# Kernel tuning notes

Measured on AMD Instinct MI355X. Metric: run time of the kernel, lower is better.

## Reference

```python
import jax, jax.numpy as jnp
import numpy as np

B, E, H = 16384, 1024, 1024


def setup_inputs() -> dict:
    key = jax.random.key(0)
    ks = jax.random.split(key, 8)
    s = 1.0 / np.sqrt(H)
    return {
        "x": jax.random.normal(ks[0], (B, E), dtype=jnp.float32),
        "h": jax.random.normal(ks[1], (B, H), dtype=jnp.float32),
        "W_ri": jax.random.normal(ks[2], (E, H), dtype=jnp.float32) * s,
        "b_ri": jnp.zeros((H,), dtype=jnp.float32),
        "W_rh": jax.random.normal(ks[3], (H, H), dtype=jnp.float32) * s,
        "W_zi": jax.random.normal(ks[4], (E, H), dtype=jnp.float32) * s,
        "b_zi": jnp.zeros((H,), dtype=jnp.float32),
        "W_zh": jax.random.normal(ks[5], (H, H), dtype=jnp.float32) * s,
        "W_hi": jax.random.normal(ks[6], (E, H), dtype=jnp.float32) * s,
        "b_hi": jnp.zeros((H,), dtype=jnp.float32),
        "W_hh": jax.random.normal(ks[7], (H, H), dtype=jnp.float32) * s,
    }


def reference(x, h, W_ri, b_ri, W_rh, W_zi, b_zi, W_zh, W_hi, b_hi, W_hh):
    # GRU cell: r/z gates then candidate htilde, then blend.
    rt = jax.nn.sigmoid(x @ W_ri + b_ri + h @ W_rh)          # [B,H]
    zt = jax.nn.sigmoid(x @ W_zi + b_zi + h @ W_zh)          # [B,H]
    htilde = jnp.tanh(x @ W_hi + b_hi + (h * rt) @ W_hh)     # [B,H]
    h_new = (1.0 - zt) * h + zt * htilde                     # [B,H]
    # dp_keep_prob=1.0 -> dropout is identity; module returns (dropout(h), h)
    return h_new
```

## Files before the change

kernel.cpp:

```cpp
#include <hip/hip_runtime.h>


typedef short bf16x8 __attribute__((ext_vector_type(8)));
typedef float f32x4 __attribute__((ext_vector_type(4)));

static __device__ __forceinline__ unsigned short f2bf(float f) {
    unsigned int u = __float_as_uint(f);
    unsigned int r = (u + 0x7fffu + ((u >> 16) & 1u)) >> 16;
    return (unsigned short)r;
}

__global__ void cast_f32_bf16(const float* __restrict__ src,
                              unsigned short* __restrict__ dst, int n) {
    int i = (blockIdx.x * blockDim.x + threadIdx.x) * 4;
    if (i < n) {
        float4 v = *(const float4*)(src + i);
        ushort4 o;
        o.x = f2bf(v.x); o.y = f2bf(v.y); o.z = f2bf(v.z); o.w = f2bf(v.w);
        *(ushort4*)(dst + i) = o;
    }
}

__global__ void transpose_cast(const float* __restrict__ src,
                               unsigned short* __restrict__ dst,
                               int dst_col_off) {
    __shared__ float t[32][33];
    int bx = blockIdx.x, by = blockIdx.y;
    int tx = threadIdx.x, ty = threadIdx.y;
#pragma unroll
    for (int i = 0; i < 4; ++i)
        t[ty + 8 * i][tx] = src[(by * 32 + ty + 8 * i) * 1024 + bx * 32 + tx];
    __syncthreads();
#pragma unroll
    for (int i = 0; i < 4; ++i) {
        int n = bx * 32 + ty + 8 * i;
        int k = by * 32 + tx;
        dst[n * 2048 + dst_col_off + k] = f2bf(t[tx][ty + 8 * i]);
    }
}

template <int MODE>
__global__ void gemm_gru(const unsigned short* __restrict__ Alo,
                         const unsigned short* __restrict__ Ahi,
                         const unsigned short* __restrict__ Bt,
                         const float* __restrict__ bias,
                         const float* __restrict__ h,
                         float* __restrict__ zt,
                         unsigned short* __restrict__ ab,
                         float* __restrict__ out) {
    __shared__ __attribute__((aligned(16))) short As[128 * 32];
    __shared__ __attribute__((aligned(16))) short Bs[128 * 32];

    const int t = threadIdx.x;
    const int lane = t & 63;
    const int wave = t >> 6;
    const int bm = blockIdx.x >> 3;
    const int bn = blockIdx.x & 7;
    const int wm = wave >> 1, wn = wave & 1;

    f32x4 acc[4][4] = {};

    const int rowA0 = bm * 128;
    const int rowB0 = bn * 128;
    const int koff = (lane >> 4) * 8;
    const int rsub = lane & 15;

    for (int k0 = 0; k0 < 2048; k0 += 32) {
        const unsigned short* Asrc = (k0 < 1024)
            ? (Alo + rowA0 * 1024 + k0)
            : (Ahi + rowA0 * 1024 + (k0 - 1024));
        const unsigned short* Bsrc = Bt + rowB0 * 2048 + k0;

        __syncthreads();
#pragma unroll
        for (int j = 0; j < 2; ++j) {
            int c = j * 256 + wave * 64 + lane;
            int row = c >> 2;
            int part = c & 3;
            __builtin_amdgcn_global_load_lds(
                (const __attribute__((address_space(1))) void*)(Asrc + row * 1024 + part * 8),
                (__attribute__((address_space(3))) void*)(As + (j * 256 + wave * 64) * 8),
                16, 0, 0);
            __builtin_amdgcn_global_load_lds(
                (const __attribute__((address_space(1))) void*)(Bsrc + row * 2048 + part * 8),
                (__attribute__((address_space(3))) void*)(Bs + (j * 256 + wave * 64) * 8),
                16, 0, 0);
        }
        __syncthreads();

        bf16x8 af[4], bfr[4];
#pragma unroll
        for (int mi = 0; mi < 4; ++mi)
            af[mi] = *(const bf16x8*)(As + (wm * 64 + mi * 16 + rsub) * 32 + koff);
#pragma unroll
        for (int ni = 0; ni < 4; ++ni)
            bfr[ni] = *(const bf16x8*)(Bs + (wn * 64 + ni * 16 + rsub) * 32 + koff);
#pragma unroll
        for (int mi = 0; mi < 4; ++mi)
#pragma unroll
            for (int ni = 0; ni < 4; ++ni)
                acc[mi][ni] = __builtin_amdgcn_mfma_f32_16x16x32_bf16(
                    af[mi], bfr[ni], acc[mi][ni], 0, 0, 0);
    }

    const int q = lane >> 4;
#pragma unroll
    for (int mi = 0; mi < 4; ++mi) {
#pragma unroll
        for (int ni = 0; ni < 4; ++ni) {
            int col = bn * 128 + wn * 64 + ni * 16 + rsub;
            int row0 = bm * 128 + wm * 64 + mi * 16 + q * 4;
            float bz = bias[col];
#pragma unroll
            for (int r = 0; r < 4; ++r) {
                int idx = (row0 + r) * 1024 + col;
                float v = acc[mi][ni][r] + bz;
                if (MODE == 0) {
                    zt[idx] = 1.0f / (1.0f + __expf(-v));
                } else if (MODE == 1) {
                    float rt = 1.0f / (1.0f + __expf(-v));
                    ab[idx] = f2bf(h[idx] * rt);
                } else {
                    float ht = tanhf(v);
                    float hv = h[idx];
                    float z = zt[idx];
                    out[idx] = fmaf(z, ht - hv, hv);
                }
            }
        }
    }
}

extern "C" void kernel_launch(void* const* d_in, const int* in_sizes, int n_in,
                              void* d_out, int out_size, void* d_ws, size_t ws_size,
                              hipStream_t stream) {
    const float* x    = (const float*)d_in[0];
    const float* h    = (const float*)d_in[1];
    const float* W_ri = (const float*)d_in[2];
    const float* b_ri = (const float*)d_in[3];
    const float* W_rh = (const float*)d_in[4];
    const float* W_zi = (const float*)d_in[5];
    const float* b_zi = (const float*)d_in[6];
    const float* W_zh = (const float*)d_in[7];
    const float* W_hi = (const float*)d_in[8];
    const float* b_hi = (const float*)d_in[9];
    const float* W_hh = (const float*)d_in[10];
    float* out = (float*)d_out;

    const size_t MB = 1024ull * 1024ull;
    char* ws = (char*)d_ws;
    unsigned short* xb  = (unsigned short*)(ws);
    unsigned short* hb  = (unsigned short*)(ws + 32 * MB);
    unsigned short* ab  = (unsigned short*)(ws + 64 * MB);
    unsigned short* WrT = (unsigned short*)(ws + 96 * MB);
    unsigned short* WzT = (unsigned short*)(ws + 100 * MB);
    unsigned short* WhT = (unsigned short*)(ws + 104 * MB);
    float* zt = (float*)(ws + 108 * MB);

    const int NELEM = 16384 * 1024;
    cast_f32_bf16<<<NELEM / (256 * 4), 256, 0, stream>>>(x, xb, NELEM);
    cast_f32_bf16<<<NELEM / (256 * 4), 256, 0, stream>>>(h, hb, NELEM);

    dim3 tb(32, 8), tg(32, 32);
    transpose_cast<<<tg, tb, 0, stream>>>(W_ri, WrT, 0);
    transpose_cast<<<tg, tb, 0, stream>>>(W_rh, WrT, 1024);
    transpose_cast<<<tg, tb, 0, stream>>>(W_zi, WzT, 0);
    transpose_cast<<<tg, tb, 0, stream>>>(W_zh, WzT, 1024);
    transpose_cast<<<tg, tb, 0, stream>>>(W_hi, WhT, 0);
    transpose_cast<<<tg, tb, 0, stream>>>(W_hh, WhT, 1024);

    gemm_gru<0><<<1024, 256, 0, stream>>>(xb, hb, WzT, b_zi, h, zt, nullptr, nullptr);
    gemm_gru<1><<<1024, 256, 0, stream>>>(xb, hb, WrT, b_ri, h, nullptr, ab, nullptr);
    gemm_gru<2><<<1024, 256, 0, stream>>>(xb, ab, WhT, b_hi, h, zt, nullptr, out);
}
```

Before: 553.3 us.

## Fuse z and r gate GEMMs with 128x256 tiles and grouped block scheduling

Merges the z and r gate GEMMs into one GEMM over a concatenated 2048-wide weight, widens the block tile to 128x256, and reorders blocks into groups of 8 M-tiles so they share B tiles. Also merges the two cast kernels and the six transpose kernels into single launches. z is now stored as bf16, r*h is computed from bf16 h, and tanh is replaced by an exp-based formula. These cut launch count, A-matrix rereads and intermediate traffic, at the cost of more registers per thread (32 accumulators) and slightly lower precision.

After: 497.5 us. -10.1%, faster.

```diff
diff --git a/kernel.cpp b/kernel.cpp
--- a/kernel.cpp
+++ b/kernel.cpp
@@ -6,25 +6,36 @@
 
 static __device__ __forceinline__ unsigned short f2bf(float f) {
     unsigned int u = __float_as_uint(f);
-    unsigned int r = (u + 0x7fffu + ((u >> 16) & 1u)) >> 16;
-    return (unsigned short)r;
-}
-
-__global__ void cast_f32_bf16(const float* __restrict__ src,
-                              unsigned short* __restrict__ dst, int n) {
+    return (unsigned short)((u + 0x7fffu + ((u >> 16) & 1u)) >> 16);
+}
+static __device__ __forceinline__ float bf2f(unsigned short s) {
+    return __uint_as_float(((unsigned int)s) << 16);
+}
+
+__global__ void cast2_f32_bf16(const float* __restrict__ a,
+                               const float* __restrict__ b,
+                               unsigned short* __restrict__ da,
+                               unsigned short* __restrict__ db, int n) {
     int i = (blockIdx.x * blockDim.x + threadIdx.x) * 4;
-    if (i < n) {
-        float4 v = *(const float4*)(src + i);
-        ushort4 o;
-        o.x = f2bf(v.x); o.y = f2bf(v.y); o.z = f2bf(v.z); o.w = f2bf(v.w);
-        *(ushort4*)(dst + i) = o;
-    }
-}
-
-__global__ void transpose_cast(const float* __restrict__ src,
-                               unsigned short* __restrict__ dst,
-                               int dst_col_off) {
+    const float* s;
+    unsigned short* d;
+    int off;
+    if (i < n) { s = a; d = da; off = i; }
+    else       { s = b; d = db; off = i - n; }
+    float4 v = *(const float4*)(s + off);
+    ushort4 o;
+    o.x = f2bf(v.x); o.y = f2bf(v.y); o.z = f2bf(v.z); o.w = f2bf(v.w);
+    *(ushort4*)(d + off) = o;
+}
+
+struct TPlan {
+    const float* src[6];
+    unsigned short* dst[6];
+};
+__global__ void transpose_cast6(TPlan p) {
     __shared__ float t[32][33];
+    const float* src = p.src[blockIdx.z];
+    unsigned short* dst = p.dst[blockIdx.z];
     int bx = blockIdx.x, by = blockIdx.y;
     int tx = threadIdx.x, ty = threadIdx.y;
 #pragma unroll
@@ -35,35 +46,52 @@
     for (int i = 0; i < 4; ++i) {
         int n = bx * 32 + ty + 8 * i;
         int k = by * 32 + tx;
-        dst[n * 2048 + dst_col_off + k] = f2bf(t[tx][ty + 8 * i]);
+        dst[n * 2048 + k] = f2bf(t[tx][ty + 8 * i]);
     }
 }
 
-template <int MODE>
-__global__ void gemm_gru(const unsigned short* __restrict__ Alo,
-                         const unsigned short* __restrict__ Ahi,
-                         const unsigned short* __restrict__ Bt,
-                         const float* __restrict__ bias,
-                         const float* __restrict__ h,
-                         float* __restrict__ zt,
-                         unsigned short* __restrict__ ab,
-                         float* __restrict__ out) {
+template <int MODE, int NBN_LOG>
+__global__ __launch_bounds__(256, 2)
+void gemm_gru(const unsigned short* __restrict__ Alo,
+              const unsigned short* __restrict__ Ahi,
+              const unsigned short* __restrict__ Bt,
+              const float* __restrict__ bias_z,
+              const float* __restrict__ bias_r,
+              const unsigned short* __restrict__ hb,
+              const unsigned short* __restrict__ ztb_in,
+              const float* __restrict__ hf,
+              unsigned short* __restrict__ ztb_out,
+              unsigned short* __restrict__ ab_out,
+              float* __restrict__ out) {
+    constexpr int NBN = 1 << NBN_LOG;
     __shared__ __attribute__((aligned(16))) short As[128 * 32];
-    __shared__ __attribute__((aligned(16))) short Bs[128 * 32];
+    __shared__ __attribute__((aligned(16))) short Bs[256 * 32];
 
     const int t = threadIdx.x;
     const int lane = t & 63;
     const int wave = t >> 6;
-    const int bm = blockIdx.x >> 3;
-    const int bn = blockIdx.x & 7;
+    const int i = blockIdx.x;
+    const int bml = i & 7;
+    const int bn = (i >> 3) & (NBN - 1);
+    const int bmg = i >> (3 + NBN_LOG);
+    const int bm = bmg * 8 + bml;
     const int wm = wave >> 1, wn = wave & 1;
 
-    f32x4 acc[4][4] = {};
+    f32x4 acc[4][8] = {};
 
     const int rowA0 = bm * 128;
-    const int rowB0 = bn * 128;
+    const int rowB0 = bn * 256;
     const int koff = (lane >> 4) * 8;
     const int rsub = lane & 15;
+
+    const short* Ap[4];
+    const short* Bp[8];
+#pragma unroll
+    for (int mi = 0; mi < 4; ++mi)
+        Ap[mi] = As + (wm * 64 + mi * 16 + rsub) * 32 + koff;
+#pragma unroll
+    for (int ni = 0; ni < 8; ++ni)
+        Bp[ni] = Bs + (wn * 128 + ni * 16 + rsub) * 32 + koff;
 
     for (int k0 = 0; k0 < 2048; k0 += 32) {
         const unsigned short* Asrc = (k0 < 1024)
@@ -75,12 +103,16 @@
 #pragma unroll
         for (int j = 0; j < 2; ++j) {
             int c = j * 256 + wave * 64 + lane;
-            int row = c >> 2;
-            int part = c & 3;
+            int row = c >> 2, part = c & 3;
             __builtin_amdgcn_global_load_lds(
                 (const __attribute__((address_space(1))) void*)(Asrc + row * 1024 + part * 8),
                 (__attribute__((address_space(3))) void*)(As + (j * 256 + wave * 64) * 8),
                 16, 0, 0);
+        }
+#pragma unroll
+        for (int j = 0; j < 4; ++j) {
+            int c = j * 256 + wave * 64 + lane;
+            int row = c >> 2, part = c & 3;
             __builtin_amdgcn_global_load_lds(
                 (const __attribute__((address_space(1))) void*)(Bsrc + row * 2048 + part * 8),
                 (__attribute__((address_space(3))) void*)(Bs + (j * 256 + wave * 64) * 8),
@@ -88,17 +120,15 @@
         }
         __syncthreads();
 
-        bf16x8 af[4], bfr[4];
+        bf16x8 af[4], bfr[8];
+#pragma unroll
+        for (int mi = 0; mi < 4; ++mi) af[mi] = *(const bf16x8*)Ap[mi];
+#pragma unroll
+        for (int ni = 0; ni < 8; ++ni) bfr[ni] = *(const bf16x8*)Bp[ni];
 #pragma unroll
         for (int mi = 0; mi < 4; ++mi)
-            af[mi] = *(const bf16x8*)(As + (wm * 64 + mi * 16 + rsub) * 32 + koff);
-#pragma unroll
-        for (int ni = 0; ni < 4; ++ni)
-            bfr[ni] = *(const bf16x8*)(Bs + (wn * 64 + ni * 16 + rsub) * 32 + koff);
-#pragma unroll
-        for (int mi = 0; mi < 4; ++mi)
-#pragma unroll
-            for (int ni = 0; ni < 4; ++ni)
+#pragma unroll
+            for (int ni = 0; ni < 8; ++ni)
                 acc[mi][ni] = __builtin_amdgcn_mfma_f32_16x16x32_bf16(
                     af[mi], bfr[ni], acc[mi][ni], 0, 0, 0);
     }
@@ -107,23 +137,32 @@
 #pragma unroll
     for (int mi = 0; mi < 4; ++mi) {
 #pragma unroll
-        for (int ni = 0; ni < 4; ++ni) {
-            int col = bn * 128 + wn * 64 + ni * 16 + rsub;
+        for (int ni = 0; ni < 8; ++ni) {
+            int colg = bn * 256 + wn * 128 + ni * 16 + rsub;
             int row0 = bm * 128 + wm * 64 + mi * 16 + q * 4;
-            float bz = bias[col];
-#pragma unroll
-            for (int r = 0; r < 4; ++r) {
-                int idx = (row0 + r) * 1024 + col;
-                float v = acc[mi][ni][r] + bz;
-                if (MODE == 0) {
-                    zt[idx] = 1.0f / (1.0f + __expf(-v));
-                } else if (MODE == 1) {
-                    float rt = 1.0f / (1.0f + __expf(-v));
-                    ab[idx] = f2bf(h[idx] * rt);
-                } else {
-                    float ht = tanhf(v);
-                    float hv = h[idx];
-                    float z = zt[idx];
+            if (MODE == 0) {
+                bool isZ = colg < 1024;
+                int col = colg & 1023;
+                float bz = isZ ? bias_z[col] : bias_r[col];
+#pragma unroll
+                for (int r = 0; r < 4; ++r) {
+                    int idx = (row0 + r) * 1024 + col;
+                    float v = acc[mi][ni][r] + bz;
+                    float s = 1.0f / (1.0f + __expf(-v));
+                    if (isZ) ztb_out[idx] = f2bf(s);
+                    else     ab_out[idx] = f2bf(bf2f(hb[idx]) * s);
+                }
+            } else {
+                int col = colg;
+                float bz = bias_z[col];
+#pragma unroll
+                for (int r = 0; r < 4; ++r) {
+                    int idx = (row0 + r) * 1024 + col;
+                    float v = acc[mi][ni][r] + bz;
+                    float e = __expf(2.0f * v);
+                    float ht = 1.0f - 2.0f / (e + 1.0f);
+                    float hv = hf[idx];
+                    float z = bf2f(ztb_in[idx]);
                     out[idx] = fmaf(z, ht - hv, hv);
                 }
             }
@@ -149,27 +188,29 @@
 
     const size_t MB = 1024ull * 1024ull;
     char* ws = (char*)d_ws;
-    unsigned short* xb  = (unsigned short*)(ws);
-    unsigned short* hb  = (unsigned short*)(ws + 32 * MB);
-    unsigned short* ab  = (unsigned short*)(ws + 64 * MB);
-    unsigned short* WrT = (unsigned short*)(ws + 96 * MB);
-    unsigned short* WzT = (unsigned short*)(ws + 100 * MB);
-    unsigned short* WhT = (unsigned short*)(ws + 104 * MB);
-    float* zt = (float*)(ws + 108 * MB);
+    unsigned short* xb   = (unsigned short*)(ws);
+    unsigned short* hb   = (unsigned short*)(ws + 32 * MB);
+    unsigned short* ab   = (unsigned short*)(ws + 64 * MB);
+    unsigned short* ztb  = (unsigned short*)(ws + 96 * MB);
+    unsigned short* Bzr  = (unsigned short*)(ws + 128 * MB);
+    unsigned short* Bh   = (unsigned short*)(ws + 136 * MB);
 
     const int NELEM = 16384 * 1024;
-    cast_f32_bf16<<<NELEM / (256 * 4), 256, 0, stream>>>(x, xb, NELEM);
-    cast_f32_bf16<<<NELEM / (256 * 4), 256, 0, stream>>>(h, hb, NELEM);
-
-    dim3 tb(32, 8), tg(32, 32);
-    transpose_cast<<<tg, tb, 0, stream>>>(W_ri, WrT, 0);
-    transpose_cast<<<tg, tb, 0, stream>>>(W_rh, WrT, 1024);
-    transpose_cast<<<tg, tb, 0, stream>>>(W_zi, WzT, 0);
-    transpose_cast<<<tg, tb, 0, stream>>>(W_zh, WzT, 1024);
-    transpose_cast<<<tg, tb, 0, stream>>>(W_hi, WhT, 0);
-    transpose_cast<<<tg, tb, 0, stream>>>(W_hh, WhT, 1024);
-
-    gemm_gru<0><<<1024, 256, 0, stream>>>(xb, hb, WzT, b_zi, h, zt, nullptr, nullptr);
-    gemm_gru<1><<<1024, 256, 0, stream>>>(xb, hb, WrT, b_ri, h, nullptr, ab, nullptr);
-    gemm_gru<2><<<1024, 256, 0, stream>>>(xb, ab, WhT, b_hi, h, zt, nullptr, out);
-}
+    cast2_f32_bf16<<<2 * NELEM / (256 * 4), 256, 0, stream>>>(x, h, xb, hb, NELEM);
+
+    TPlan p;
+    p.src[0] = W_zi; p.dst[0] = Bzr + 0 * 2048 + 0;
+    p.src[1] = W_zh; p.dst[1] = Bzr + 0 * 2048 + 1024;
+    p.src[2] = W_ri; p.dst[2] = Bzr + 1024 * 2048 + 0;
+    p.src[3] = W_rh; p.dst[3] = Bzr + 1024 * 2048 + 1024;
+    p.src[4] = W_hi; p.dst[4] = Bh + 0;
+    p.src[5] = W_hh; p.dst[5] = Bh + 1024;
+    transpose_cast6<<<dim3(32, 32, 6), dim3(32, 8), 0, stream>>>(p);
+
+    gemm_gru<0, 3><<<1024, 256, 0, stream>>>(xb, hb, Bzr, b_zi, b_ri,
+                                             hb, nullptr, nullptr,
+                                             ztb, ab, nullptr);
+    gemm_gru<1, 2><<<512, 256, 0, stream>>>(xb, ab, Bh, b_hi, nullptr,
+                                            nullptr, ztb, h,
+                                            nullptr, nullptr, out);
+}
```
